# Kernel tuning notes

Measured on AMD Instinct MI355X. Metric: run time of the kernel, lower is better.

Reference implementation:

```python
import jax, jax.numpy as jnp
import numpy as np

B, T, C, H = 32, 1024, 384, 64

def setup_inputs() -> dict:
    key = jax.random.key(0)
    k1, k2, k3, k4 = jax.random.split(key, 4)
    x = jax.random.normal(k1, (B, T, C), dtype=jnp.float32)
    s = 1.0 / np.sqrt(C)
    Wk = jax.random.normal(k2, (C, H), dtype=jnp.float32) * s
    Wq = jax.random.normal(k3, (C, H), dtype=jnp.float32) * s
    Wv = jax.random.normal(k4, (C, H), dtype=jnp.float32) * s
    return {"x": x, "Wk": Wk, "Wq": Wq, "Wv": Wv}

def reference(x, Wk, Wq, Wv):
    # Single-head causal attention (dropout = identity, eval mode).
    Tn = x.shape[1]
    k = jnp.einsum('btc,ch->bth', x, Wk)   # [B,T,H]
    q = jnp.einsum('btc,ch->bth', x, Wq)
    v = jnp.einsum('btc,ch->bth', x, Wv)
    scale = k.shape[-1] ** -0.5
    wei = jnp.einsum('bth,bsh->bts', q, k) * scale  # [B,T,T]
    causal = jnp.tril(jnp.ones((Tn, Tn), dtype=bool))
    wei = jnp.where(causal, wei, -jnp.inf)
    wei = jax.nn.softmax(wei, axis=-1)
    out = jnp.einsum('bts,bsh->bth', wei, v)  # [B,T,H]
    return out
```

## Files before the change

### kernel.cpp

```cpp
#include <hip/hip_runtime.h>
#include <hip/hip_bf16.h>

#define BB 32
#define TT 1024
#define CCH 384
#define HH 64

typedef short short8 __attribute__((ext_vector_type(8)));
typedef float f32x4 __attribute__((ext_vector_type(4)));
typedef unsigned short ushort;

static __device__ __forceinline__ ushort f2bf(float f) {
    union { __hip_bfloat16 h; ushort u; } v;
    v.h = __float2bfloat16(f);
    return v.u;
}

__global__ void wswz(const float* __restrict__ Wk, const float* __restrict__ Wq,
                     const float* __restrict__ Wv, ushort* __restrict__ wf) {
    const int mat = blockIdx.x, ks = blockIdx.y;
    const float* W = (mat == 0) ? Wk : ((mat == 1) ? Wq : Wv);
    const int t = threadIdx.x;
    const int ct = t >> 6, lane = t & 63, quad = lane >> 4, l15 = lane & 15;
    const int col = ct * 16 + l15;
    short8 d;
#pragma unroll
    for (int j = 0; j < 8; ++j)
        d[j] = (short)f2bf(W[(ks * 32 + quad * 8 + j) * 64 + col]);
    *(short8*)(wf + (((mat * 12 + ks) * 4 + ct) << 9) + lane * 8) = d;
}

#define XSTR 388
#define VS_STRIDE 66

__global__ __launch_bounds__(256, 2) void qkv(const float* __restrict__ x,
                                              const ushort* __restrict__ wf,
                                              ushort* __restrict__ kb,
                                              ushort* __restrict__ qb,
                                              ushort* __restrict__ vtb) {
    const int r0 = blockIdx.x * 64;
    const int tid = threadIdx.x;
    const int wv = tid >> 6, lane = tid & 63, l15 = lane & 15, quad = lane >> 4;

    __shared__ ushort xs[64 * XSTR];

#pragma unroll
    for (int kb3 = 0; kb3 < 3; ++kb3) {
        const int kbase = kb3 * 128;
        const int seg = (tid & 7) * 16;
#pragma unroll
        for (int i = 0; i < 2; ++i) {
            const int r = (tid >> 3) + 32 * i;
            const float* src = x + (size_t)(r0 + r) * CCH + kbase + seg;
            f32x4 v0 = *(const f32x4*)(src);
            f32x4 v1 = *(const f32x4*)(src + 4);
            f32x4 v2 = *(const f32x4*)(src + 8);
            f32x4 v3 = *(const f32x4*)(src + 12);
            short8 p0, p1;
#pragma unroll
            for (int j = 0; j < 4; ++j) {
                p0[j]     = (short)f2bf(v0[j]);
                p0[j + 4] = (short)f2bf(v1[j]);
                p1[j]     = (short)f2bf(v2[j]);
                p1[j + 4] = (short)f2bf(v3[j]);
            }
            *(short8*)(xs + r * XSTR + kbase + seg) = p0;
            *(short8*)(xs + r * XSTR + kbase + seg + 8) = p1;
        }
    }
    __syncthreads();

    f32x4 acc[12] = {};
    short8 bf[2][12];
#pragma unroll
    for (int m = 0; m < 3; ++m)
#pragma unroll
        for (int ct = 0; ct < 4; ++ct)
            bf[0][m * 4 + ct] = *(const short8*)(wf + (((m * 12 + 0) * 4 + ct) << 9) + lane * 8);

#pragma unroll
    for (int ks = 0; ks < 12; ++ks) {
        short8 a = *(const short8*)(xs + (wv * 16 + l15) * XSTR + ks * 32 + quad * 8);
        if (ks < 11) {
#pragma unroll
            for (int m = 0; m < 3; ++m)
#pragma unroll
                for (int ct = 0; ct < 4; ++ct)
                    bf[(ks + 1) & 1][m * 4 + ct] =
                        *(const short8*)(wf + (((m * 12 + ks + 1) * 4 + ct) << 9) + lane * 8);
        }
#pragma unroll
        for (int f = 0; f < 12; ++f)
            acc[f] = __builtin_amdgcn_mfma_f32_16x16x32_bf16(a, bf[ks & 1][f], acc[f], 0, 0, 0);
    }

#pragma unroll
    for (int ct = 0; ct < 4; ++ct) {
#pragma unroll
        for (int r = 0; r < 4; ++r) {
            int row = r0 + wv * 16 + quad * 4 + r;
            int col = ct * 16 + l15;
            kb[row * 64 + col] = f2bf(acc[0 + ct][r]);
            qb[row * 64 + col] = f2bf(acc[4 + ct][r]);
        }
    }
    __syncthreads();
    ushort* vs = xs;
#pragma unroll
    for (int ct = 0; ct < 4; ++ct)
#pragma unroll
        for (int r = 0; r < 4; ++r)
            vs[(wv * 16 + quad * 4 + r) * VS_STRIDE + ct * 16 + l15] = f2bf(acc[8 + ct][r]);
    __syncthreads();
    {
        const int col = tid >> 2;
        const int rbase = (tid & 3) * 16;
        short8 d0, d1;
#pragma unroll
        for (int j = 0; j < 8; ++j) {
            d0[j] = (short)vs[(rbase + j) * VS_STRIDE + col];
            d1[j] = (short)vs[(rbase + 8 + j) * VS_STRIDE + col];
        }
        const int b = r0 >> 10;
        const int t = (r0 & 1023) + rbase;
        *(short8*)(vtb + b * 65536 + col * 1024 + t) = d0;
        *(short8*)(vtb + b * 65536 + col * 1024 + t + 8) = d1;
    }
}

#define PSTR2 40
#define KSTR 72
#define VSTR 136

__global__ __launch_bounds__(256, 3) void attn(const ushort* __restrict__ qb,
                                               const ushort* __restrict__ kb,
                                               const ushort* __restrict__ vtb,
                                               float* __restrict__ out) {
    const int y = blockIdx.y;
    int qt;
    if (y < 8)       qt = 31 - y;
    else if (y < 16) qt = y - 8;
    else if (y < 24) qt = 39 - y;
    else             qt = y - 16;
    const int b = blockIdx.x;
    const int t0 = qt * 32;
    const int tid = threadIdx.x;
    const int w = tid >> 6, lane = tid & 63, l15 = lane & 15, quad = lane >> 4;

    __shared__ __align__(16) char arena[46080];
    ushort* Ks = (ushort*)arena;
    ushort* Vs = (ushort*)(arena + 18432);
    ushort* Ps = (ushort*)(arena + 35840);
    ushort* Psw = Ps + w * 32 * PSTR2;

    const ushort* kbb = kb  + (size_t)b * 65536;
    const ushort* vbb = vtb + (size_t)b * 65536;

    short8 qf0[2], qf1[2];
#pragma unroll
    for (int m = 0; m < 2; ++m) {
        const int qrow = b * 1024 + t0 + m * 16 + l15;
        qf0[m] = *(const short8*)(qb + qrow * 64 + quad * 8);
        qf1[m] = *(const short8*)(qb + qrow * 64 + 32 + quad * 8);
    }

    f32x4 o[2][4] = {};
    float li[2][4] = {};
    const float c1 = 0.125f * 1.4426950408889634f;
    const float c2 = 10.0f * 1.4426950408889634f;

    const int nst = (qt >> 2) + 1;

    short8 kr[4], vr[4];
#pragma unroll
    for (int i = 0; i < 4; ++i) {
        int c = tid + i * 256;
        kr[i] = *(const short8*)(kbb + (c >> 3) * 64 + (c & 7) * 8);
        vr[i] = *(const short8*)(vbb + (c >> 4) * 1024 + (c & 15) * 8);
    }

    for (int it = 0; it < nst; ++it) {
        const int s0 = it * 128;
        __syncthreads();
#pragma unroll
        for (int i = 0; i < 4; ++i) {
            int c = tid + i * 256;
            *(short8*)(Ks + (c >> 3) * KSTR + (c & 7) * 8) = kr[i];
            *(short8*)(Vs + (c >> 4) * VSTR + (c & 15) * 8) = vr[i];
        }
        __syncthreads();
        if (it + 1 < nst) {
            const int sn = s0 + 128;
#pragma unroll
            for (int i = 0; i < 4; ++i) {
                int c = tid + i * 256;
                kr[i] = *(const short8*)(kbb + (sn + (c >> 3)) * 64 + (c & 7) * 8);
                vr[i] = *(const short8*)(vbb + (c >> 4) * 1024 + sn + (c & 15) * 8);
            }
        }

        f32x4 s[2][2];
        __builtin_amdgcn_s_setprio(1);
#pragma unroll
        for (int g = 0; g < 2; ++g) {
            const ushort* kp = Ks + (w * 32 + g * 16 + l15) * KSTR + quad * 8;
            short8 b0 = *(const short8*)(kp);
            short8 b1 = *(const short8*)(kp + 32);
#pragma unroll
            for (int m = 0; m < 2; ++m) {
                f32x4 z = {};
                z = __builtin_amdgcn_mfma_f32_16x16x32_bf16(qf0[m], b0, z, 0, 0, 0);
                s[m][g] = __builtin_amdgcn_mfma_f32_16x16x32_bf16(qf1[m], b1, z, 0, 0, 0);
            }
        }
        __builtin_amdgcn_s_setprio(0);

        if (it + 1 < nst) {
#pragma unroll
            for (int m = 0; m < 2; ++m)
#pragma unroll
                for (int g = 0; g < 2; ++g)
#pragma unroll
                    for (int r = 0; r < 4; ++r) {
                        float p = exp2f(s[m][g][r] * c1 - c2);
                        li[m][r] += p;
                        Psw[(m * 16 + quad * 4 + r) * PSTR2 + g * 16 + l15] = f2bf(p);
                    }
        } else {
#pragma unroll
            for (int m = 0; m < 2; ++m)
#pragma unroll
                for (int g = 0; g < 2; ++g)
#pragma unroll
                    for (int r = 0; r < 4; ++r) {
                        const int trow = t0 + m * 16 + quad * 4 + r;
                        const int col = s0 + w * 32 + g * 16 + l15;
                        float p = (col <= trow) ? exp2f(s[m][g][r] * c1 - c2) : 0.f;
                        li[m][r] += p;
                        Psw[(m * 16 + quad * 4 + r) * PSTR2 + g * 16 + l15] = f2bf(p);
                    }
        }

        short8 pa[2];
#pragma unroll
        for (int m = 0; m < 2; ++m)
            pa[m] = *(const short8*)(Psw + (m * 16 + l15) * PSTR2 + quad * 8);

        __builtin_amdgcn_s_setprio(1);
        short8 vbf[4];
#pragma unroll
        for (int ct = 0; ct < 4; ++ct)
            vbf[ct] = *(const short8*)(Vs + (ct * 16 + l15) * VSTR + w * 32 + quad * 8);
#pragma unroll
        for (int m = 0; m < 2; ++m)
#pragma unroll
            for (int ct = 0; ct < 4; ++ct)
                o[m][ct] = __builtin_amdgcn_mfma_f32_16x16x32_bf16(pa[m], vbf[ct], o[m][ct], 0, 0, 0);
        __builtin_amdgcn_s_setprio(0);
    }

    __syncthreads();

#pragma unroll
    for (int m = 0; m < 2; ++m)
#pragma unroll
        for (int r = 0; r < 4; ++r) {
            float rs = li[m][r];
#pragma unroll
            for (int off = 1; off < 16; off <<= 1)
                rs += __shfl_xor(rs, off);
            li[m][r] = rs;
        }

    float* slotO = (float*)arena;
    float* slotL = (float*)(arena + 34816);
#pragma unroll
    for (int m = 0; m < 2; ++m) {
        const int sl = w * 2 + m;
#pragma unroll
        for (int ct = 0; ct < 4; ++ct)
#pragma unroll
            for (int r = 0; r < 4; ++r)
                slotO[(sl * 4 + ct) * 272 + (quad * 4 + r) * 17 + l15] = o[m][ct][r];
        if (l15 == 0)
#pragma unroll
            for (int r = 0; r < 4; ++r)
                slotL[sl * 16 + quad * 4 + r] = li[m][r];
    }
    __syncthreads();

    {
        const int mh = w >> 1, cb = (w & 1) * 2;
#pragma unroll
        for (int r = 0; r < 4; ++r) {
            float lsum = 0.f;
#pragma unroll
            for (int wp = 0; wp < 4; ++wp)
                lsum += slotL[(wp * 2 + mh) * 16 + quad * 4 + r];
            const float inv = 1.0f / lsum;
            const int t = t0 + mh * 16 + quad * 4 + r;
#pragma unroll
            for (int cc = 0; cc < 2; ++cc) {
                const int ct = cb + cc;
                float v = 0.f;
#pragma unroll
                for (int wp = 0; wp < 4; ++wp)
                    v += slotO[((wp * 2 + mh) * 4 + ct) * 272 + (quad * 4 + r) * 17 + l15];
                out[b * 65536 + t * 64 + ct * 16 + l15] = v * inv;
            }
        }
    }
}

extern "C" void kernel_launch(void* const* d_in, const int* in_sizes, int n_in,
                              void* d_out, int out_size, void* d_ws, size_t ws_size,
                              hipStream_t stream) {
    const float* x  = (const float*)d_in[0];
    const float* Wk = (const float*)d_in[1];
    const float* Wq = (const float*)d_in[2];
    const float* Wv = (const float*)d_in[3];

    char* ws = (char*)d_ws;
    ushort* wf  = (ushort*)ws;
    ushort* kb  = (ushort*)(ws + 256 * 1024);
    ushort* qb  = (ushort*)(ws + 256 * 1024 + 4u * 1024 * 1024);
    ushort* vtb = (ushort*)(ws + 256 * 1024 + 8u * 1024 * 1024);

    wswz<<<dim3(3, 12), dim3(256), 0, stream>>>(Wk, Wq, Wv, wf);
    qkv<<<dim3(512), dim3(256), 0, stream>>>(x, wf, kb, qb, vtb);
    attn<<<dim3(32, 32), dim3(256), 0, stream>>>(qb, kb, vtb, (float*)d_out);
}
```

Before: 119.8 us.

## Process query subtiles sequentially to shrink P buffer and raise occupancy

The attention loop now handles the two 16-row query subtiles one at a time. Each subtile computes its scores, exponentiates, stages P through LDS and accumulates P·V before the next subtile starts. Each wave's P staging area is halved, so the shared arena drops from 46080 to 40960 bytes, and launch bounds rise from 3 to 4 blocks per CU. The aim is to cut LDS and register pressure so more waves stay resident and hide latency. The cost is more serialisation inside each wave, fewer independent MFMAs in flight, and possible register spills under the tighter bound.

```diff
diff --git a/kernel.cpp b/kernel.cpp
--- a/kernel.cpp
+++ b/kernel.cpp
@@ -132,7 +132,7 @@
 #define KSTR 72
 #define VSTR 136
 
-__global__ __launch_bounds__(256, 3) void attn(const ushort* __restrict__ qb,
+__global__ __launch_bounds__(256, 4) void attn(const ushort* __restrict__ qb,
                                                const ushort* __restrict__ kb,
                                                const ushort* __restrict__ vtb,
                                                float* __restrict__ out) {
@@ -147,11 +147,11 @@
     const int tid = threadIdx.x;
     const int w = tid >> 6, lane = tid & 63, l15 = lane & 15, quad = lane >> 4;
 
-    __shared__ __align__(16) char arena[46080];
+    __shared__ __align__(16) char arena[40960];
     ushort* Ks = (ushort*)arena;
     ushort* Vs = (ushort*)(arena + 18432);
     ushort* Ps = (ushort*)(arena + 35840);
-    ushort* Psw = Ps + w * 32 * PSTR2;
+    ushort* Psw = Ps + w * 16 * PSTR2;
 
     const ushort* kbb = kb  + (size_t)b * 65536;
     const ushort* vbb = vtb + (size_t)b * 65536;
@@ -199,64 +199,58 @@
             }
         }
 
-        f32x4 s[2][2];
-        __builtin_amdgcn_s_setprio(1);
+        short8 kb0[2], kb1[2];
 #pragma unroll
         for (int g = 0; g < 2; ++g) {
             const ushort* kp = Ks + (w * 32 + g * 16 + l15) * KSTR + quad * 8;
-            short8 b0 = *(const short8*)(kp);
-            short8 b1 = *(const short8*)(kp + 32);
-#pragma unroll
-            for (int m = 0; m < 2; ++m) {
+            kb0[g] = *(const short8*)(kp);
+            kb1[g] = *(const short8*)(kp + 32);
+        }
+
+#pragma unroll
+        for (int m = 0; m < 2; ++m) {
+            f32x4 s[2];
+            __builtin_amdgcn_s_setprio(1);
+#pragma unroll
+            for (int g = 0; g < 2; ++g) {
                 f32x4 z = {};
-                z = __builtin_amdgcn_mfma_f32_16x16x32_bf16(qf0[m], b0, z, 0, 0, 0);
-                s[m][g] = __builtin_amdgcn_mfma_f32_16x16x32_bf16(qf1[m], b1, z, 0, 0, 0);
-            }
-        }
-        __builtin_amdgcn_s_setprio(0);
-
-        if (it + 1 < nst) {
-#pragma unroll
-            for (int m = 0; m < 2; ++m)
+                z = __builtin_amdgcn_mfma_f32_16x16x32_bf16(qf0[m], kb0[g], z, 0, 0, 0);
+                s[g] = __builtin_amdgcn_mfma_f32_16x16x32_bf16(qf1[m], kb1[g], z, 0, 0, 0);
+            }
+            __builtin_amdgcn_s_setprio(0);
+
+            if (it + 1 < nst) {
 #pragma unroll
                 for (int g = 0; g < 2; ++g)
 #pragma unroll
                     for (int r = 0; r < 4; ++r) {
-                        float p = exp2f(s[m][g][r] * c1 - c2);
+                        float p = exp2f(s[g][r] * c1 - c2);
                         li[m][r] += p;
-                        Psw[(m * 16 + quad * 4 + r) * PSTR2 + g * 16 + l15] = f2bf(p);
+                        Psw[(quad * 4 + r) * PSTR2 + g * 16 + l15] = f2bf(p);
                     }
-        } else {
-#pragma unroll
-            for (int m = 0; m < 2; ++m)
+            } else {
 #pragma unroll
                 for (int g = 0; g < 2; ++g)
 #pragma unroll
                     for (int r = 0; r < 4; ++r) {
                         const int trow = t0 + m * 16 + quad * 4 + r;
                         const int col = s0 + w * 32 + g * 16 + l15;
-                        float p = (col <= trow) ? exp2f(s[m][g][r] * c1 - c2) : 0.f;
+                        float p = (col <= trow) ? exp2f(s[g][r] * c1 - c2) : 0.f;
                         li[m][r] += p;
-                        Psw[(m * 16 + quad * 4 + r) * PSTR2 + g * 16 + l15] = f2bf(p);
+                        Psw[(quad * 4 + r) * PSTR2 + g * 16 + l15] = f2bf(p);
                     }
-        }
-
-        short8 pa[2];
-#pragma unroll
-        for (int m = 0; m < 2; ++m)
-            pa[m] = *(const short8*)(Psw + (m * 16 + l15) * PSTR2 + quad * 8);
-
-        __builtin_amdgcn_s_setprio(1);
-        short8 vbf[4];
-#pragma unroll
-        for (int ct = 0; ct < 4; ++ct)
-            vbf[ct] = *(const short8*)(Vs + (ct * 16 + l15) * VSTR + w * 32 + quad * 8);
-#pragma unroll
-        for (int m = 0; m < 2; ++m)
-#pragma unroll
-            for (int ct = 0; ct < 4; ++ct)
-                o[m][ct] = __builtin_amdgcn_mfma_f32_16x16x32_bf16(pa[m], vbf[ct], o[m][ct], 0, 0, 0);
-        __builtin_amdgcn_s_setprio(0);
+            }
+
+            short8 pa = *(const short8*)(Psw + l15 * PSTR2 + quad * 8);
+
+            __builtin_amdgcn_s_setprio(1);
+#pragma unroll
+            for (int ct = 0; ct < 4; ++ct) {
+                short8 vbf = *(const short8*)(Vs + (ct * 16 + l15) * VSTR + w * 32 + quad * 8);
+                o[m][ct] = __builtin_amdgcn_mfma_f32_16x16x32_bf16(pa, vbf, o[m][ct], 0, 0, 0);
+            }
+            __builtin_amdgcn_s_setprio(0);
+        }
     }
 
     __syncthreads();
```

Result: slower. 155.8 us (+30.0%).
